# Performance work log

Measured on AMD Instinct MI355X. Metric: run time of the kernel, lower is better.

Reference implementation:

```python
import jax, jax.numpy as jnp
import numpy as np

B, S, D = 4, 2048, 2048
H, HD = 16, 128
MAX_SEQ = 2048


def setup_inputs() -> dict:
    key = jax.random.key(0)
    ks = jax.random.split(key, 6)
    scale = 1.0 / np.sqrt(D)
    h = jax.random.normal(ks[0], (B, S, D), dtype=jnp.float32)
    Wq = jax.random.normal(ks[1], (D, H * HD), dtype=jnp.float32) * scale
    Wk = jax.random.normal(ks[2], (D, H * HD), dtype=jnp.float32) * scale
    Wv = jax.random.normal(ks[3], (D, H * HD), dtype=jnp.float32) * scale
    Wo = jax.random.normal(ks[4], (H * HD, D), dtype=jnp.float32) * scale
    # torch Linear stores weight as [out, in]; keep that layout
    Wq, Wk, Wv, Wo = Wq.T, Wk.T, Wv.T, Wo.T
    K_cache = jnp.zeros((B, H, MAX_SEQ, HD), dtype=jnp.float32)
    V_cache = jnp.zeros((B, H, MAX_SEQ, HD), dtype=jnp.float32)
    # standard RoPE angles: theta = pos / 10000^(2i/hd)
    inv_freq = 1.0 / (10000.0 ** (np.arange(0, HD, 2, dtype=np.float32) / HD))
    t = np.arange(MAX_SEQ, dtype=np.float32)
    ang = np.outer(t, inv_freq)  # [MAX_SEQ, HD//2]
    freqs_cos = jnp.asarray(np.cos(ang), dtype=jnp.float32)
    freqs_sin = jnp.asarray(np.sin(ang), dtype=jnp.float32)
    return {"h": h, "Wq": Wq, "Wk": Wk, "Wv": Wv, "Wo": Wo,
            "K_cache": K_cache, "V_cache": V_cache,
            "freqs_cos": freqs_cos, "freqs_sin": freqs_sin, "pos": 0}


def _rope(x, cos, sin):
    # x: [B,H,S,HD]; cos/sin: [1,1,S,HD//2]; complex multiply on (even,odd) pairs
    xr = x.reshape(*x.shape[:-1], -1, 2)
    x0, x1 = xr[..., 0], xr[..., 1]
    out = jnp.stack([x0 * cos - x1 * sin, x0 * sin + x1 * cos], axis=-1)
    return out.reshape(x.shape)


def reference(h, Wq, Wk, Wv, Wo, K_cache, V_cache, freqs_cos, freqs_sin, pos):
    Bq, Sq, _ = h.shape
    Q = jnp.einsum('bsd,ed->bse', h, Wq).reshape(Bq, Sq, H, HD).transpose(0, 2, 1, 3)
    K = jnp.einsum('bsd,ed->bse', h, Wk).reshape(Bq, Sq, H, HD).transpose(0, 2, 1, 3)
    V = jnp.einsum('bsd,ed->bse', h, Wv).reshape(Bq, Sq, H, HD).transpose(0, 2, 1, 3)
    cos = freqs_cos[pos:pos + Sq][None, None]
    sin = freqs_sin[pos:pos + Sq][None, None]
    Q = _rope(Q, cos, sin)
    K = _rope(K, cos, sin)
    # KV-cache append then read back prefix
    K_full = jax.lax.dynamic_update_slice(K_cache, K, (0, 0, pos, 0))
    V_full = jax.lax.dynamic_update_slice(V_cache, V, (0, 0, pos, 0))
    L = pos + Sq
    K_all = K_full[:, :, :L]
    V_all = V_full[:, :, :L]
    scores = jnp.einsum('bhqd,bhkd->bhqk', Q, K_all) / jnp.sqrt(jnp.float32(HD))
    if Sq > 1:  # causal: query at absolute position pos+i attends keys <= pos+i
        mask = (pos + jnp.arange(Sq))[:, None] >= jnp.arange(L)[None, :]
        scores = jnp.where(mask[None, None], scores, jnp.float32(-1e30))
    attn = jax.nn.softmax(scores, axis=-1)
    out = jnp.einsum('bhqk,bhkd->bhqd', attn, V_all)
    out = out.transpose(0, 2, 1, 3).reshape(Bq, Sq, H * HD)
    return jnp.einsum('bse,de->bsd', out, Wo)
```

## Files before the change

### kernel.cpp

```cpp
#include <hip/hip_runtime.h>
#include <hip/hip_bf16.h>

typedef __attribute__((ext_vector_type(8))) short bf16x8;
typedef __attribute__((ext_vector_type(4))) float f32x4;
typedef __attribute__((ext_vector_type(4))) unsigned short u16x4;

#define BB 4
#define SS 2048
#define DD 2048
#define HH 16
#define HDD 128
#define MASKV (-30000.0f)
#define MINIT (-15000.0f)

__device__ __forceinline__ unsigned short f2bf(float f) {
  __hip_bfloat16 b = __float2bfloat16(f);
  return *reinterpret_cast<unsigned short*>(&b);
}
__device__ __forceinline__ void gl_lds16(const void* g, void* l) {
  __builtin_amdgcn_global_load_lds((const __attribute__((address_space(1))) unsigned int*)g,
                                   (__attribute__((address_space(3))) unsigned int*)l, 16, 0, 0);
}

__global__ __launch_bounds__(256) void convertk(const float* __restrict__ src,
                                                __hip_bfloat16* __restrict__ dst, int n4) {
  int i = blockIdx.x * 256 + threadIdx.x;
  if (i >= n4) return;
  f32x4 v = ((const f32x4*)src)[i];
  u16x4 o;
  o[0] = f2bf(v[0]); o[1] = f2bf(v[1]); o[2] = f2bf(v[2]); o[3] = f2bf(v[3]);
  ((u16x4*)dst)[i] = o;
}

template <int MODE>
__global__ __launch_bounds__(512, 1) void gemm256(const __hip_bfloat16* __restrict__ A,
                                                  const __hip_bfloat16* __restrict__ Bw,
                                                  __hip_bfloat16* __restrict__ Cbf,
                                                  __hip_bfloat16* __restrict__ Vt,
                                                  float* __restrict__ Cf,
                                                  const float* __restrict__ fc,
                                                  const float* __restrict__ fs,
                                                  const int* __restrict__ posp,
                                                  int M, int N, int K) {
  __shared__ __hip_bfloat16 As[2][2][128 * 64];
  __shared__ __hip_bfloat16 Bs[2][2][128 * 64];
  const int tid = threadIdx.x;
  const int wid = tid >> 6, lane = tid & 63;
  const int l15 = lane & 15, l4 = lane >> 4;
  const int wm = wid >> 2, wn = wid & 3;

  const int nbn = N >> 8;
  const int nb = (M >> 8) * nbn;
  const int bid = blockIdx.x;
  const int swz = (bid & 7) * (nb >> 3) + (bid >> 3);
  const int bm = swz / nbn, bn = swz % nbn;

  const int NT = K >> 6;

#define STAGE_HALF(Q, BUF, K0G)                                                   \
  {                                                                               \
    if ((Q) < 2) {                                                                \
      const long rowb = (long)bm * 256 + (Q) * 128;                               \
      _Pragma("unroll") for (int i = 0; i < 2; i++) {                             \
        int c = i * 512 + tid, rr = c >> 3, jj = (c & 7) ^ (rr & 7);              \
        gl_lds16(A + (rowb + rr) * (long)K + (K0G) + jj * 8,                      \
                 &As[BUF][(Q)][0] + c * 8);                                       \
      }                                                                           \
    } else {                                                                      \
      const long rowb = (long)bn * 256 + ((Q) - 2) * 128;                         \
      _Pragma("unroll") for (int i = 0; i < 2; i++) {                             \
        int c = i * 512 + tid, rr = c >> 3, jj = (c & 7) ^ (rr & 7);              \
        gl_lds16(Bw + (rowb + rr) * (long)K + (K0G) + jj * 8,                     \
                 &Bs[BUF][(Q) - 2][0] + c * 8);                                   \
      }                                                                           \
    }                                                                             \
  }

  f32x4 acc[8][4] = {};

#pragma unroll
  for (int q = 0; q < 4; ++q) STAGE_HALF(q, 0, 0);
#pragma unroll
  for (int q = 0; q < 4; ++q) STAGE_HALF(q, 1, 64);
  __syncthreads();

  for (int T = 0; T < NT; ++T) {
    const int cur = T & 1;
    const int nxt = cur ^ 1;
    const bool do_stage = (T >= 1) && (T + 1 < NT);
    const int k0n = (T + 1) << 6;

#pragma unroll
    for (int k2 = 0; k2 < 2; ++k2) {
      bf16x8 af[8], bg[4];
#pragma unroll
      for (int mi = 0; mi < 8; mi++) {
        int r = mi * 16 + l15;
        int j = (k2 * 4 + l4) ^ (r & 7);
        af[mi] = *(const bf16x8*)(&As[cur][wm][0] + r * 64 + j * 8);
      }
#pragma unroll
      for (int ni = 0; ni < 4; ni++) {
        int r = (wn & 1) * 64 + ni * 16 + l15;
        int j = (k2 * 4 + l4) ^ (r & 7);
        bg[ni] = *(const bf16x8*)(&Bs[cur][wn >> 1][0] + r * 64 + j * 8);
      }
      if (do_stage) {
        if (k2 == 0) { STAGE_HALF(0, nxt, k0n); STAGE_HALF(1, nxt, k0n); }
        else         { STAGE_HALF(2, nxt, k0n); STAGE_HALF(3, nxt, k0n); }
      }
      __builtin_amdgcn_s_barrier();
      asm volatile("" ::: "memory");
      __builtin_amdgcn_s_setprio(1);
#pragma unroll
      for (int mi = 0; mi < 8; mi++)
#pragma unroll
        for (int ni = 0; ni < 4; ni++)
          acc[mi][ni] = __builtin_amdgcn_mfma_f32_16x16x32_bf16(af[mi], bg[ni],
                                                                acc[mi][ni], 0, 0, 0);
      __builtin_amdgcn_s_setprio(0);
      if (k2 == 1) asm volatile("s_waitcnt vmcnt(0)" ::: "memory");
      __builtin_amdgcn_s_barrier();
      asm volatile("" ::: "memory");
    }
  }
#undef STAGE_HALF

  if (MODE == 0) {
    if (bn * 256 < 4096) {
      const int pos = *posp;
#pragma unroll
      for (int mi = 0; mi < 8; mi++)
#pragma unroll
        for (int ni = 0; ni < 4; ni++) {
          int n = bn * 256 + wn * 64 + ni * 16 + l15;
          int hd = n & 127;
          int ip = hd >> 1;
          bool odd = hd & 1;
#pragma unroll
          for (int r = 0; r < 4; r++) {
            float v = acc[mi][ni][r];
            float p = __shfl_xor(v, 1, 64);
            int m = bm * 256 + wm * 128 + mi * 16 + l4 * 4 + r;
            int s = m & (SS - 1);
            float cv = fc[(long)(pos + s) * 64 + ip];
            float sv = fs[(long)(pos + s) * 64 + ip];
            float out = odd ? (p * sv + v * cv) : (v * cv - p * sv);
            Cbf[(long)m * 4096 + n] = __float2bfloat16(out);
          }
        }
    } else {
#pragma unroll
      for (int mi = 0; mi < 8; mi++)
#pragma unroll
        for (int ni = 0; ni < 4; ni++) {
          int e = bn * 256 + wn * 64 + ni * 16 + l15 - 4096;
          int hh = e >> 7, hd = e & 127;
          int m0 = bm * 256 + wm * 128 + mi * 16 + l4 * 4;
          int b = m0 >> 11, s0 = m0 & (SS - 1);
          u16x4 pk;
#pragma unroll
          for (int r = 0; r < 4; r++) pk[r] = f2bf(acc[mi][ni][r]);
          *(u16x4*)(Vt + (((long)(b * HH + hh) * 128 + hd) * SS + s0)) = pk;
        }
    }
  } else {
#pragma unroll
    for (int mi = 0; mi < 8; mi++)
#pragma unroll
      for (int ni = 0; ni < 4; ni++) {
        int n = bn * 256 + wn * 64 + ni * 16 + l15;
#pragma unroll
        for (int r = 0; r < 4; r++) {
          int m = bm * 256 + wm * 128 + mi * 16 + l4 * 4 + r;
          Cf[(long)m * N + n] = acc[mi][ni][r];
        }
      }
  }
}

__global__ __launch_bounds__(256, 2) void attn_k(const __hip_bfloat16* __restrict__ qk,
                                                 const __hip_bfloat16* __restrict__ vt,
                                                 __hip_bfloat16* __restrict__ aout,
                                                 const int* __restrict__ posp) {
  __shared__ __hip_bfloat16 Ks[64 * 128];
  __shared__ __hip_bfloat16 Vs[128 * 64];
  __shared__ __hip_bfloat16 Ps[4][16 * 64];
  const int pos = *posp;
  const int orig = blockIdx.x;
  const int swz = (orig & 7) * 128 + (orig >> 3);
  const int qp = swz & 15, bh = swz >> 4;
  const int b = bh >> 4, h = bh & 15;
  const int tid = threadIdx.x;
  const int wave = tid >> 6, lane = tid & 63;
  const int l15 = lane & 15, l4 = lane >> 4;

  const long kbase = ((long)b * SS) * 4096 + 2048 + h * 128;
  const long vbase = ((long)bh * 128) * SS;
  const float sc2 = 0.08838834764831845f * 1.4426950408889634f;

  const int s_kr[4] = {(0 * 256 + tid) >> 4, (1 * 256 + tid) >> 4, (2 * 256 + tid) >> 4, (3 * 256 + tid) >> 4};
  const int s_kc = tid & 15;
  const int s_hd[4] = {(0 * 256 + tid) >> 3, (1 * 256 + tid) >> 3, (2 * 256 + tid) >> 3, (3 * 256 + tid) >> 3};
  const int s_vc = tid & 7;

  bf16x8 kreg[4], vreg[4];

#define LOADKV(T)                                                                             \
  {                                                                                           \
    const int kv0_ = (T) * 64;                                                                \
    _Pragma("unroll") for (int i = 0; i < 4; i++) {                                           \
      kreg[i] = *(const bf16x8*)(qk + kbase + (long)(kv0_ + s_kr[i]) * 4096 + s_kc * 8);      \
      vreg[i] = *(const bf16x8*)(vt + vbase + (long)s_hd[i] * SS + kv0_ + s_vc * 8);          \
    }                                                                                         \
  }

#define STAGE()                                                                               \
  {                                                                                           \
    _Pragma("unroll") for (int i = 0; i < 4; i++) {                                           \
      *(bf16x8*)(Ks + ((s_kr[i] * 128 + s_kc * 8) ^ ((s_kr[i] & 7) << 3))) = kreg[i];         \
      *(bf16x8*)(Vs + ((s_hd[i] * 64 + s_vc * 8) ^ ((s_hd[i] & 7) << 3))) = vreg[i];          \
    }                                                                                         \
  }

  for (int half = 0; half < 2; ++half) {
    const int qb = half ? (31 - qp) : qp;
    const int qwb = qb * 64 + wave * 16;

    bf16x8 qf[4];
#pragma unroll
    for (int kk = 0; kk < 4; kk++) {
      long row = (long)b * SS + qwb + l15;
      qf[kk] = *(const bf16x8*)(qk + row * 4096 + h * 128 + kk * 32 + l4 * 8);
    }

    f32x4 accO[8] = {};
    float mrun[4], lrun[4];
#pragma unroll
    for (int r = 0; r < 4; r++) { mrun[r] = MINIT; lrun[r] = 0.f; }

    int ntiles = (pos + qb * 64 + 63) / 64 + 1;
    if (ntiles > SS / 64) ntiles = SS / 64;
#define TT(t) (half ? (ntiles - 1 - (t)) : (t))

    LOADKV(TT(0));
    __syncthreads();
    STAGE();

    for (int t = 0; t < ntiles; ++t) {
      const int kv0 = TT(t) * 64;
      __syncthreads();
      if (t + 1 < ntiles) LOADKV(TT(t + 1));

      f32x4 sfr[4] = {};
      __builtin_amdgcn_s_setprio(1);
#pragma unroll
      for (int ni = 0; ni < 4; ni++) {
        const int key = ni * 16 + l15;
        const int sw = (key & 7) << 3;
#pragma unroll
        for (int kk = 0; kk < 4; kk++) {
          bf16x8 kf = *(const bf16x8*)(Ks + ((key * 128 + kk * 32 + l4 * 8) ^ sw));
          sfr[ni] = __builtin_amdgcn_mfma_f32_16x16x32_bf16(qf[kk], kf, sfr[ni], 0, 0, 0);
        }
      }
      __builtin_amdgcn_s_setprio(0);

      const bool needmask = (kv0 + 63) > (pos + qb * 64);
#pragma unroll
      for (int ni = 0; ni < 4; ni++)
#pragma unroll
        for (int r = 0; r < 4; r++) {
          float v = sfr[ni][r] * sc2;
          if (needmask) {
            int key = kv0 + ni * 16 + l15;
            int q = qwb + l4 * 4 + r;
            if (key > pos + q) v = MASKV;
          }
          sfr[ni][r] = v;
        }

      {
        f32x4 mx = sfr[0];
#pragma unroll
        for (int ni = 1; ni < 4; ni++)
#pragma unroll
          for (int r = 0; r < 4; r++) mx[r] = fmaxf(mx[r], sfr[ni][r]);
#pragma unroll
        for (int d = 1; d < 16; d <<= 1)
#pragma unroll
          for (int r = 0; r < 4; r++) mx[r] = fmaxf(mx[r], __shfl_xor(mx[r], d, 64));

        float growth = mx[0] - mrun[0];
#pragma unroll
        for (int r = 1; r < 4; r++) growth = fmaxf(growth, mx[r] - mrun[r]);
        if (!__all(growth <= 11.0f)) {
          float scal[4];
#pragma unroll
          for (int r = 0; r < 4; r++) {
            float mn = fmaxf(mrun[r], mx[r]);
            scal[r] = exp2f(mrun[r] - mn);
            mrun[r] = mn;
            lrun[r] *= scal[r];
          }
#pragma unroll
          for (int ni = 0; ni < 8; ni++)
#pragma unroll
            for (int r = 0; r < 4; r++) accO[ni][r] *= scal[r];
        }

        f32x4 rs = {0.f, 0.f, 0.f, 0.f};
#pragma unroll
        for (int ni = 0; ni < 4; ni++)
#pragma unroll
          for (int r = 0; r < 4; r++) {
            float p = exp2f(sfr[ni][r] - mrun[r]);
            rs[r] += p;
            int prow = l4 * 4 + r;
            Ps[wave][(prow * 64 + ni * 16 + l15) ^ ((prow & 7) << 3)] = __float2bfloat16(p);
          }
#pragma unroll
        for (int d = 1; d < 16; d <<= 1)
#pragma unroll
          for (int r = 0; r < 4; r++) rs[r] += __shfl_xor(rs[r], d, 64);
#pragma unroll
        for (int r = 0; r < 4; r++) lrun[r] += rs[r];
      }

      __builtin_amdgcn_s_setprio(1);
#pragma unroll
      for (int kk = 0; kk < 2; kk++) {
        int prow = l15;
        bf16x8 pf = *(const bf16x8*)(Ps[wave] + ((prow * 64 + kk * 32 + l4 * 8) ^ ((prow & 7) << 3)));
#pragma unroll
        for (int ni = 0; ni < 8; ni++) {
          int hd = ni * 16 + l15;
          bf16x8 vf = *(const bf16x8*)(Vs + ((hd * 64 + kk * 32 + l4 * 8) ^ ((hd & 7) << 3)));
          accO[ni] = __builtin_amdgcn_mfma_f32_16x16x32_bf16(pf, vf, accO[ni], 0, 0, 0);
        }
      }
      __builtin_amdgcn_s_setprio(0);

      __syncthreads();
      if (t + 1 < ntiles) STAGE();
    }
#undef TT

    __hip_bfloat16* E = Ks + wave * 2048;
    {
      float inv[4];
#pragma unroll
      for (int r = 0; r < 4; r++) inv[r] = 1.0f / lrun[r];
#pragma unroll
      for (int ni = 0; ni < 8; ni++)
#pragma unroll
        for (int r = 0; r < 4; r++) {
          int row = l4 * 4 + r;
          E[(row * 128 + ni * 16 + l15) ^ ((row & 7) << 3)] =
              __float2bfloat16(accO[ni][r] * inv[r]);
        }
    }
    const long gb = ((long)b * SS + qwb) * 2048 + h * 128;
#pragma unroll
    for (int j = 0; j < 4; j++) {
      int row = j * 4 + l4;
      int c8 = l15 * 8;
      bf16x8 v = *(const bf16x8*)(E + ((row * 128 + c8) ^ ((row & 7) << 3)));
      *(bf16x8*)(aout + gb + (long)row * 2048 + c8) = v;
    }
  }
#undef LOADKV
#undef STAGE
}

extern "C" void kernel_launch(void* const* d_in, const int* in_sizes, int n_in,
                              void* d_out, int out_size, void* d_ws, size_t ws_size,
                              hipStream_t stream) {
  (void)in_sizes; (void)n_in; (void)out_size; (void)ws_size;
  const float* h  = (const float*)d_in[0];
  const float* Wq = (const float*)d_in[1];
  const float* Wk = (const float*)d_in[2];
  const float* Wv = (const float*)d_in[3];
  const float* Wo = (const float*)d_in[4];
  const float* fc = (const float*)d_in[7];
  const float* fs = (const float*)d_in[8];
  const int* pos  = (const int*)d_in[9];
  float* out = (float*)d_out;

  char* ws = (char*)d_ws;
  __hip_bfloat16* hb    = (__hip_bfloat16*)(ws);
  __hip_bfloat16* wqkv  = (__hip_bfloat16*)(ws + 33554432);
  __hip_bfloat16* wo_b  = (__hip_bfloat16*)(ws + 58720256);
  __hip_bfloat16* qkbuf = (__hip_bfloat16*)(ws + 67108864);
  __hip_bfloat16* vt    = (__hip_bfloat16*)(ws + 134217728);
  __hip_bfloat16* aout  = hb;

  convertk<<<16384, 256, 0, stream>>>(h, hb, 4194304);
  convertk<<<4096, 256, 0, stream>>>(Wq, wqkv, 1048576);
  convertk<<<4096, 256, 0, stream>>>(Wk, wqkv + 4194304, 1048576);
  convertk<<<4096, 256, 0, stream>>>(Wv, wqkv + 8388608, 1048576);
  convertk<<<4096, 256, 0, stream>>>(Wo, wo_b, 1048576);

  gemm256<0><<<768, 512, 0, stream>>>(hb, wqkv, qkbuf, vt, nullptr, fc, fs, pos,
                                      8192, 6144, 2048);

  attn_k<<<1024, 256, 0, stream>>>(qkbuf, vt, aout, pos);

  gemm256<1><<<256, 512, 0, stream>>>(aout, wo_b, nullptr, nullptr, out, nullptr,
                                      nullptr, nullptr, 8192, 2048, 2048);
}
```

Measured before the change: 487.5 us.

## Switch GEMM to 4-stage K=32 LDS ring with counted vmcnt waits

Restructures the bf16 GEMM main loop from a double-buffered K=64 tile, split into two half-steps, into a 4-buffer ring of K=32 tiles with a prefetch distance of two. The LDS swizzle changes to match 32-wide rows. Each iteration issues its loads and then waits with a partial vmcnt count, so only the oldest tile must have landed, and uses one barrier instead of two. The aim is to keep more global loads in flight and cut sync overhead. The cost is fewer MFMAs per barrier, and since no barrier follows compute, there is a possible race on buffer reuse.

Measured after the change: 505.0 us. +3.6%, slower.

```diff
diff --git a/kernel.cpp b/kernel.cpp
--- a/kernel.cpp
+++ b/kernel.cpp
@@ -42,8 +42,8 @@
                                                   const float* __restrict__ fs,
                                                   const int* __restrict__ posp,
                                                   int M, int N, int K) {
-  __shared__ __hip_bfloat16 As[2][2][128 * 64];
-  __shared__ __hip_bfloat16 Bs[2][2][128 * 64];
+  __shared__ __hip_bfloat16 As[4][256 * 32];
+  __shared__ __hip_bfloat16 Bs[4][256 * 32];
   const int tid = threadIdx.x;
   const int wid = tid >> 6, lane = tid & 63;
   const int l15 = lane & 15, l4 = lane >> 4;
@@ -55,76 +55,58 @@
   const int swz = (bid & 7) * (nb >> 3) + (bid >> 3);
   const int bm = swz / nbn, bn = swz % nbn;
 
-  const int NT = K >> 6;
-
-#define STAGE_HALF(Q, BUF, K0G)                                                   \
+  const int NT = K >> 5;
+
+#define STAGE_TILE(TT, BUF)                                                       \
   {                                                                               \
-    if ((Q) < 2) {                                                                \
-      const long rowb = (long)bm * 256 + (Q) * 128;                               \
-      _Pragma("unroll") for (int i = 0; i < 2; i++) {                             \
-        int c = i * 512 + tid, rr = c >> 3, jj = (c & 7) ^ (rr & 7);              \
-        gl_lds16(A + (rowb + rr) * (long)K + (K0G) + jj * 8,                      \
-                 &As[BUF][(Q)][0] + c * 8);                                       \
-      }                                                                           \
-    } else {                                                                      \
-      const long rowb = (long)bn * 256 + ((Q) - 2) * 128;                         \
-      _Pragma("unroll") for (int i = 0; i < 2; i++) {                             \
-        int c = i * 512 + tid, rr = c >> 3, jj = (c & 7) ^ (rr & 7);              \
-        gl_lds16(Bw + (rowb + rr) * (long)K + (K0G) + jj * 8,                     \
-                 &Bs[BUF][(Q) - 2][0] + c * 8);                                   \
-      }                                                                           \
+    const int k0_ = (TT) << 5;                                                    \
+    _Pragma("unroll") for (int i = 0; i < 2; i++) {                               \
+      int c = i * 512 + tid, rr = c >> 2, jj = (c & 3) ^ ((rr >> 1) & 3);         \
+      gl_lds16(A + ((long)bm * 256 + rr) * K + k0_ + jj * 8,                      \
+               &As[BUF][0] + c * 8);                                              \
+      gl_lds16(Bw + ((long)bn * 256 + rr) * K + k0_ + jj * 8,                     \
+               &Bs[BUF][0] + c * 8);                                              \
     }                                                                             \
   }
 
   f32x4 acc[8][4] = {};
 
-#pragma unroll
-  for (int q = 0; q < 4; ++q) STAGE_HALF(q, 0, 0);
-#pragma unroll
-  for (int q = 0; q < 4; ++q) STAGE_HALF(q, 1, 64);
-  __syncthreads();
+  STAGE_TILE(0, 0);
+  STAGE_TILE(1, 1);
 
   for (int T = 0; T < NT; ++T) {
-    const int cur = T & 1;
-    const int nxt = cur ^ 1;
-    const bool do_stage = (T >= 1) && (T + 1 < NT);
-    const int k0n = (T + 1) << 6;
-
-#pragma unroll
-    for (int k2 = 0; k2 < 2; ++k2) {
-      bf16x8 af[8], bg[4];
-#pragma unroll
-      for (int mi = 0; mi < 8; mi++) {
-        int r = mi * 16 + l15;
-        int j = (k2 * 4 + l4) ^ (r & 7);
-        af[mi] = *(const bf16x8*)(&As[cur][wm][0] + r * 64 + j * 8);
-      }
-#pragma unroll
-      for (int ni = 0; ni < 4; ni++) {
-        int r = (wn & 1) * 64 + ni * 16 + l15;
-        int j = (k2 * 4 + l4) ^ (r & 7);
-        bg[ni] = *(const bf16x8*)(&Bs[cur][wn >> 1][0] + r * 64 + j * 8);
-      }
-      if (do_stage) {
-        if (k2 == 0) { STAGE_HALF(0, nxt, k0n); STAGE_HALF(1, nxt, k0n); }
-        else         { STAGE_HALF(2, nxt, k0n); STAGE_HALF(3, nxt, k0n); }
-      }
-      __builtin_amdgcn_s_barrier();
-      asm volatile("" ::: "memory");
-      __builtin_amdgcn_s_setprio(1);
-#pragma unroll
-      for (int mi = 0; mi < 8; mi++)
-#pragma unroll
-        for (int ni = 0; ni < 4; ni++)
-          acc[mi][ni] = __builtin_amdgcn_mfma_f32_16x16x32_bf16(af[mi], bg[ni],
-                                                                acc[mi][ni], 0, 0, 0);
-      __builtin_amdgcn_s_setprio(0);
-      if (k2 == 1) asm volatile("s_waitcnt vmcnt(0)" ::: "memory");
-      __builtin_amdgcn_s_barrier();
-      asm volatile("" ::: "memory");
-    }
-  }
-#undef STAGE_HALF
+    const int cb = T & 3;
+    if (T + 2 < NT) STAGE_TILE(T + 2, (T + 2) & 3);
+
+    if (T + 2 < NT)      asm volatile("s_waitcnt vmcnt(8)" ::: "memory");
+    else if (T + 1 < NT) asm volatile("s_waitcnt vmcnt(4)" ::: "memory");
+    else                 asm volatile("s_waitcnt vmcnt(0)" ::: "memory");
+    __builtin_amdgcn_s_barrier();
+    asm volatile("" ::: "memory");
+
+    bf16x8 af[8], bg[4];
+#pragma unroll
+    for (int ni = 0; ni < 4; ni++) {
+      int r = wn * 64 + ni * 16 + l15;
+      int j = l4 ^ ((r >> 1) & 3);
+      bg[ni] = *(const bf16x8*)(&Bs[cb][0] + r * 32 + j * 8);
+    }
+#pragma unroll
+    for (int mi = 0; mi < 8; mi++) {
+      int r = wm * 128 + mi * 16 + l15;
+      int j = l4 ^ ((r >> 1) & 3);
+      af[mi] = *(const bf16x8*)(&As[cb][0] + r * 32 + j * 8);
+    }
+    __builtin_amdgcn_s_setprio(1);
+#pragma unroll
+    for (int mi = 0; mi < 8; mi++)
+#pragma unroll
+      for (int ni = 0; ni < 4; ni++)
+        acc[mi][ni] = __builtin_amdgcn_mfma_f32_16x16x32_bf16(af[mi], bg[ni],
+                                                              acc[mi][ni], 0, 0, 0);
+    __builtin_amdgcn_s_setprio(0);
+  }
+#undef STAGE_TILE
 
   if (MODE == 0) {
     if (bn * 256 < 4096) {
```
